# Kernel optimization log

Measured on AMD Instinct MI355X. Metric: run time of the kernel, lower is better.

The kernel has to match this reference:

```python
import jax, jax.numpy as jnp
import numpy as np

MAX_DISP = 4  # max_displacement; window = (2*MAX_DISP+1)**2 = 81 displacements


def setup_inputs() -> dict:
    key = jax.random.key(0)
    k1, k2 = jax.random.split(key)
    B, C, H, W = 8, 128, 128, 128
    in1 = jax.random.normal(k1, (B, C, H, W), dtype=jnp.float32)
    in2 = jax.random.normal(k2, (B, C, H, W), dtype=jnp.float32)
    return {"in1": in1, "in2": in2}


def reference(in1, in2):
    # Cost-volume correlation (kernel_size=1): for each displacement (dy,dx) in
    # [-d, d]^2, corr[b, w, y, x] = mean_c in1[b,c,y,x] * in2_pad[b,c,y+dy,x+dx],
    # matching torch unfold ordering: w = dy_idx*(2d+1) + dx_idx (row-major).
    B, C, H, W = in1.shape
    d = MAX_DISP
    in2_pad = jnp.pad(in2, ((0, 0), (0, 0), (d, d), (d, d)))  # zero pad, like ConstantPad2d
    corr = [
        jnp.mean(in1 * jax.lax.slice(in2_pad, (0, 0, dy, dx), (B, C, dy + H, dx + W)), axis=1)
        for dy in range(2 * d + 1)
        for dx in range(2 * d + 1)
    ]
    return jnp.stack(corr, axis=1)  # [B, (2d+1)^2, H, W]
```

## Files before the change

kernel.cpp:

```cpp
#include <hip/hip_runtime.h>


#define MAXD 4
#define ND 9
#define NDISP 81
#define BATCH 8
#define CH 128
#define HH 128
#define WW 128
#define HW (HH * WW)
#define NCHUNK CH
#define TY 4
#define NT 576

__device__ __forceinline__ float dpp_shr1(float x) {
    return __int_as_float(__builtin_amdgcn_update_dpp(
        0, __float_as_int(x), 0x111, 0xF, 0xF, true));
}
__device__ __forceinline__ float dpp_shl1(float x) {
    return __int_as_float(__builtin_amdgcn_update_dpp(
        0, __float_as_int(x), 0x101, 0xF, 0xF, true));
}

__global__ __launch_bounds__(NT, 1) void corr_kernel(
    const float* __restrict__ in1,
    const float* __restrict__ in2,
    float* __restrict__ out)
{
    const int tid = threadIdx.x;
    const int b   = blockIdx.x;
    const int y0  = blockIdx.y * TY;
    const int xg  = tid & 15;
    const int dy  = (tid >> 4) % ND;
    const int ly  = tid / 144;
    const int rl  = ly + dy;
    const bool rok = (unsigned)(y0 + rl - MAXD) < (unsigned)HH;
    int r2 = y0 + rl - MAXD;
    r2 = r2 < 0 ? 0 : (r2 > HH - 1 ? HH - 1 : r2);

    const float* p2 = in2 + (size_t)b * CH * HW + (size_t)r2 * WW + xg * 8;
    const float* p1 = in1 + (size_t)b * CH * HW + (size_t)(y0 + ly) * WW + xg * 8;

    float acc[ND][8];
    #pragma unroll
    for (int d = 0; d < ND; ++d)
        #pragma unroll
        for (int i = 0; i < 8; ++i) acc[d][i] = 0.0f;

    float w0[8], a0[8], w1[8], a1[8];

    auto LD = [&](float* w, float* a) {
        float4 t0 = *(const float4*)(p2);
        float4 t1 = *(const float4*)(p2 + 4);
        float4 u0 = *(const float4*)(p1);
        float4 u1 = *(const float4*)(p1 + 4);
        w[0] = t0.x; w[1] = t0.y; w[2] = t0.z; w[3] = t0.w;
        w[4] = t1.x; w[5] = t1.y; w[6] = t1.z; w[7] = t1.w;
        a[0] = u0.x; a[1] = u0.y; a[2] = u0.z; a[3] = u0.w;
        a[4] = u1.x; a[5] = u1.y; a[6] = u1.z; a[7] = u1.w;
        p2 += HW; p1 += HW;
    };

    auto CMP = [&](const float* w, const float* a) {
        float W[16];
        W[0]  = dpp_shr1(w[4]);
        W[1]  = dpp_shr1(w[5]);
        W[2]  = dpp_shr1(w[6]);
        W[3]  = dpp_shr1(w[7]);
        #pragma unroll
        for (int i = 0; i < 8; ++i) W[4 + i] = w[i];
        W[12] = dpp_shl1(w[0]);
        W[13] = dpp_shl1(w[1]);
        W[14] = dpp_shl1(w[2]);
        W[15] = dpp_shl1(w[3]);
        #pragma unroll
        for (int d = 0; d < ND; ++d)
            #pragma unroll
            for (int i = 0; i < 8; ++i)
                acc[d][i] = fmaf(a[i], W[i + d], acc[d][i]);
    };

    LD(w0, a0);
    #pragma unroll 1
    for (int k = 0; k < NCHUNK; k += 2) {
        LD(w1, a1);
        CMP(w0, a0);
        if (k + 2 < NCHUNK) LD(w0, a0);
        CMP(w1, a1);
    }

    const float sc = rok ? (1.0f / (float)CH) : 0.0f;
    float* outb = out + (size_t)b * NDISP * HW
                      + (size_t)(y0 + ly) * WW + xg * 8;
    #pragma unroll
    for (int d = 0; d < ND; ++d) {
        float* op = outb + (size_t)(dy * ND + d) * HW;
        float4 v0 = make_float4(acc[d][0] * sc, acc[d][1] * sc,
                                acc[d][2] * sc, acc[d][3] * sc);
        float4 v1 = make_float4(acc[d][4] * sc, acc[d][5] * sc,
                                acc[d][6] * sc, acc[d][7] * sc);
        *(float4*)(op)     = v0;
        *(float4*)(op + 4) = v1;
    }
}

extern "C" void kernel_launch(void* const* d_in, const int* in_sizes, int n_in,
                              void* d_out, int out_size, void* d_ws, size_t ws_size,
                              hipStream_t stream) {
    const float* in1 = (const float*)d_in[0];
    const float* in2 = (const float*)d_in[1];
    float* out = (float*)d_out;
    dim3 grid(BATCH, HH / TY);
    corr_kernel<<<grid, NT, 0, stream>>>(in1, in2, out);
}
```

Baseline: 192.8 us.

## Stage in1 rows through double-buffered LDS loaded by one wave

In the old code every thread re-read its in1 row from global memory, so each in1 value was loaded 9 times across the dy groups. Now wave 0 prefetches two channels of the block's 4 in1 rows into a double-buffered shared-memory array, and all threads read their in1 operands from LDS. The cost is a workgroup barrier every two channels and a single wave carrying the whole in1 load, which may serialize progress across the 9 waves.

```diff
diff --git a/kernel.cpp b/kernel.cpp
--- a/kernel.cpp
+++ b/kernel.cpp
@@ -22,11 +22,16 @@
         0, __float_as_int(x), 0x101, 0xF, 0xF, true));
 }
 
+#define PUBBAR() asm volatile( \
+    "s_waitcnt lgkmcnt(0)\n\ts_barrier" ::: "memory")
+
 __global__ __launch_bounds__(NT, 1) void corr_kernel(
     const float* __restrict__ in1,
     const float* __restrict__ in2,
     float* __restrict__ out)
 {
+    __shared__ float s1[2][2][TY * WW];
+
     const int tid = threadIdx.x;
     const int b   = blockIdx.x;
     const int y0  = blockIdx.y * TY;
@@ -39,7 +44,12 @@
     r2 = r2 < 0 ? 0 : (r2 > HH - 1 ? HH - 1 : r2);
 
     const float* p2 = in2 + (size_t)b * CH * HW + (size_t)r2 * WW + xg * 8;
-    const float* p1 = in1 + (size_t)b * CH * HW + (size_t)(y0 + ly) * WW + xg * 8;
+
+    const int wv   = __builtin_amdgcn_readfirstlane(tid >> 6);
+    const int lane = tid & 63;
+    const float* p1w = in1 + (size_t)b * CH * HW + (size_t)y0 * WW + lane * 8;
+
+    const int aoff = ly * WW + xg * 8;
 
     float acc[ND][8];
     #pragma unroll
@@ -47,20 +57,22 @@
         #pragma unroll
         for (int i = 0; i < 8; ++i) acc[d][i] = 0.0f;
 
-    float w0[8], a0[8], w1[8], a1[8];
+    float w0[8], w1[8];
 
-    auto LD = [&](float* w, float* a) {
+    auto LDW = [&](float* w) {
         float4 t0 = *(const float4*)(p2);
         float4 t1 = *(const float4*)(p2 + 4);
-        float4 u0 = *(const float4*)(p1);
-        float4 u1 = *(const float4*)(p1 + 4);
         w[0] = t0.x; w[1] = t0.y; w[2] = t0.z; w[3] = t0.w;
         w[4] = t1.x; w[5] = t1.y; w[6] = t1.z; w[7] = t1.w;
+        p2 += HW;
+    };
+    auto LDA = [&](int c, float* a) {
+        const float* ap = &s1[(c >> 1) & 1][c & 1][aoff];
+        float4 u0 = *(const float4*)(ap);
+        float4 u1 = *(const float4*)(ap + 4);
         a[0] = u0.x; a[1] = u0.y; a[2] = u0.z; a[3] = u0.w;
         a[4] = u1.x; a[5] = u1.y; a[6] = u1.z; a[7] = u1.w;
-        p2 += HW; p1 += HW;
     };
-
     auto CMP = [&](const float* w, const float* a) {
         float W[16];
         W[0]  = dpp_shr1(w[4]);
@@ -80,13 +92,54 @@
                 acc[d][i] = fmaf(a[i], W[i + d], acc[d][i]);
     };
 
-    LD(w0, a0);
+    if (wv == 0) {
+        const float* g0 = p1w;
+        const float* g1 = p1w + HW;
+        float4 t0 = *(const float4*)(g0);
+        float4 t1 = *(const float4*)(g0 + 4);
+        float4 t2 = *(const float4*)(g1);
+        float4 t3 = *(const float4*)(g1 + 4);
+        float* l0 = &s1[0][0][lane * 8];
+        *(float4*)(l0)     = t0;
+        *(float4*)(l0 + 4) = t1;
+        float* l1 = &s1[0][1][lane * 8];
+        *(float4*)(l1)     = t2;
+        *(float4*)(l1 + 4) = t3;
+    }
+    LDW(w0);
+    PUBBAR();
+
     #pragma unroll 1
     for (int k = 0; k < NCHUNK; k += 2) {
-        LD(w1, a1);
-        CMP(w0, a0);
-        if (k + 2 < NCHUNK) LD(w0, a0);
-        CMP(w1, a1);
+        const bool pf = (k + 2 < NCHUNK);
+        float4 t0, t1, t2, t3;
+        if (wv == 0 && pf) {
+            const float* g0 = p1w + (size_t)(k + 2) * HW;
+            const float* g1 = p1w + (size_t)(k + 3) * HW;
+            t0 = *(const float4*)(g0);
+            t1 = *(const float4*)(g0 + 4);
+            t2 = *(const float4*)(g1);
+            t3 = *(const float4*)(g1 + 4);
+        }
+
+        float A0[8], A1[8];
+        LDA(k, A0);
+        LDA(k + 1, A1);
+        LDW(w1);
+        CMP(w0, A0);
+        if (pf) LDW(w0);
+        CMP(w1, A1);
+
+        if (wv == 0 && pf) {
+            const int nb = ((k + 2) >> 1) & 1;
+            float* l0 = &s1[nb][0][lane * 8];
+            *(float4*)(l0)     = t0;
+            *(float4*)(l0 + 4) = t1;
+            float* l1 = &s1[nb][1][lane * 8];
+            *(float4*)(l1)     = t2;
+            *(float4*)(l1 + 4) = t3;
+        }
+        PUBBAR();
     }
 
     const float sc = rok ? (1.0f / (float)CH) : 0.0f;
```

Result: slower. 206.4 us (+7.0%).
